# Performance work log

Measured on AMD Instinct MI355X. Metric: run time of the kernel, lower is better.

## Reference

```python
import jax, jax.numpy as jnp
import numpy as np

LMBD = 0.1      # cfg['MODEL']['LAMBDA'][0]
MU = 0.1        # ISTA/FISTA step size (cfg['MODEL']['MU'])
N_STEPS = 4     # cfg['MODEL']['NUM_LAYERS']
FISTA = True    # cfg['MODEL']['ISFISTA']


def _conv(x, W, s, p):
    # torch F.conv2d, NCHW / OIHW
    return jax.lax.conv_general_dilated(x, W, (s, s), [(p, p), (p, p)],
        dimension_numbers=('NCHW', 'OIHW', 'NCHW'))


def _conv_t(z, W, s, p):
    # torch F.conv_transpose2d(z, W, stride=s, padding=p): output (H-1)*s + k - 2p
    k = W.shape[-1]
    Wt = jnp.transpose(jnp.flip(W, (-2, -1)), (1, 0, 2, 3))
    pad = k - 1 - p
    return jax.lax.conv_general_dilated(z, Wt, (1, 1), [(pad, pad), (pad, pad)],
        lhs_dilation=(s, s), dimension_numbers=('NCHW', 'OIHW', 'NCHW'))


def _wnorm(W):
    # per-atom unit-norm dictionary (w_norm=True)
    return W / (jnp.sqrt(jnp.sum(W * W, axis=(1, 2, 3), keepdims=True)) + 1e-12)


def _dict_block(x, W, s, p):
    # unrolled FISTA sparse coding: min_z 0.5||x - W^T*z||^2 + lmbd||z||_1, z>=0
    thr = MU * LMBD
    shrink = lambda u: jax.nn.relu(u - thr)  # non-negative soft threshold
    z0 = shrink(MU * _conv(x, W, s, p))

    def body(carry, _):
        z, z_old, t = carry
        if FISTA:
            t_new = (1.0 + jnp.sqrt(1.0 + 4.0 * t * t)) * 0.5
            y = z + ((t - 1.0) / t_new) * (z - z_old)
        else:
            t_new, y = t, z
        r = x - _conv_t(y, W, s, p)                 # residual in image space
        z_new = shrink(y + MU * _conv(r, W, s, p))  # gradient step + shrinkage
        return (z_new, z, t_new), None

    (z, _, _), _ = jax.lax.scan(body, (z0, z0, jnp.float32(1.0)), None, length=N_STEPS - 1)
    return z


def _bn(x, eps=1e-5):
    # BatchNorm2d at init (gamma=1, beta=0), training-mode batch stats, biased var
    m = jnp.mean(x, axis=(0, 2, 3), keepdims=True)
    v = jnp.var(x, axis=(0, 2, 3), keepdims=True)
    return (x - m) * jax.lax.rsqrt(v + eps)


def _lrelu(x):
    return jnp.where(x >= 0, x, 0.2 * x)


def setup_inputs() -> dict:
    key = jax.random.key(0)
    ks = jax.random.split(key, 7)
    nc, ndf, nz = 3, 64, 128

    def kaiming(k, shape):
        fan_in = shape[1] * shape[2] * shape[3]
        bound = float(np.sqrt(6.0 / fan_in))
        return jax.random.uniform(k, shape, jnp.float32, -bound, bound)

    return {
        'x':  jax.random.normal(ks[0], (64, nc, 96, 96), jnp.float32),
        'W1': kaiming(ks[1], (ndf, nc, 4, 4)),
        'W2': kaiming(ks[2], (ndf * 2, ndf, 4, 4)),
        'W3': kaiming(ks[3], (ndf * 4, ndf * 2, 4, 4)),
        'W4': kaiming(ks[4], (ndf * 8, ndf * 4, 4, 4)),
        'W5': kaiming(ks[5], (ndf * 16, ndf * 8, 4, 4)),
        'W6': kaiming(ks[6], (nz, ndf * 16, 3, 3)),
    }


def reference(x, W1, W2, W3, W4, W5, W6):
    Ws = [_wnorm(w) for w in (W1, W2, W3, W4, W5, W6)]
    # encoder: 96 -> 48 -> 24 -> 12 -> 6 -> 3 -> 1
    o = _lrelu(_dict_block(x, Ws[0], 2, 1))
    for i in range(1, 5):
        o = _lrelu(_bn(_dict_block(o, Ws[i], 2, 1)))
    z = _dict_block(o, Ws[5], 1, 0).reshape(x.shape[0], -1)
    z = z / jnp.maximum(jnp.linalg.norm(z, axis=1, keepdims=True), 1e-12)  # F.normalize
    # decoder (DictConv2d.inverse chain, uses the normalized dictionaries)
    h = z.reshape(z.shape[0], -1, 1, 1)
    h = jax.nn.relu(_bn(_conv_t(h, Ws[5], 1, 0)))
    for i in (4, 3, 2, 1):
        h = jax.nn.relu(_bn(_conv_t(h, Ws[i], 2, 1)))
    x_hat = jnp.tanh(_conv_t(h, Ws[0], 2, 1))
    return z, x_hat
```

## Files before the change

### kernel.cpp

```cpp
#include <hip/hip_runtime.h>
#include <math.h>

#define BLK 256
static constexpr float MU_F  = 0.1f;
static constexpr float THR_F = 0.01f;

typedef __attribute__((ext_vector_type(8))) short bf16x8;
typedef __attribute__((ext_vector_type(4))) float f32x4;

__device__ inline unsigned short f2bf(float f) {
    unsigned u = __float_as_uint(f);
    unsigned r = (u + 0x7fffu + ((u >> 16) & 1u)) >> 16;
    return (unsigned short)r;
}
__device__ inline float bf2f(unsigned short h) {
    return __uint_as_float(((unsigned)h) << 16);
}

__device__ inline float blk_reduce(float v) {
    __shared__ float sh[BLK];
    int tid = threadIdx.x;
    sh[tid] = v;
    __syncthreads();
    #pragma unroll
    for (int s = BLK / 2; s > 0; s >>= 1) {
        if (tid < s) sh[tid] += sh[tid + s];
        __syncthreads();
    }
    float r = sh[0];
    __syncthreads();
    return r;
}

__global__ __launch_bounds__(BLK) void wnorm_pack(
    const float* __restrict__ W, float* __restrict__ Wkc,
    float* __restrict__ Wnout, int Mout, int asz)
{
    int o = blockIdx.x;
    const float* w = W + (size_t)o * asz;
    float s = 0.f;
    for (int i = threadIdx.x; i < asz; i += BLK) { float v = w[i]; s = fmaf(v, v, s); }
    float tot = blk_reduce(s);
    float inv = 1.0f / (sqrtf(tot) + 1e-12f);
    for (int i = threadIdx.x; i < asz; i += BLK) {
        float v = w[i] * inv;
        Wkc[(size_t)i * Mout + o] = v;
        if (Wnout) Wnout[(size_t)o * asz + i] = v;
    }
}

__global__ __launch_bounds__(BLK) void wnorm_pack_bf16(
    const float* __restrict__ W, short* __restrict__ Cpk, short* __restrict__ Tpk,
    int Cout, int Cin)
{
    int o = blockIdx.x;
    int asz = Cin * 16;
    const float* w = W + (size_t)o * asz;
    float s = 0.f;
    for (int i = threadIdx.x; i < asz; i += BLK) { float v = w[i]; s = fmaf(v, v, s); }
    float tot = blk_reduce(s);
    float inv = 1.0f / (sqrtf(tot) + 1e-12f);
    size_t cTot = (size_t)Cout * asz;
    size_t parStride = (size_t)Cout * 4 * Cin;
    size_t tTot = 4 * parStride;
    for (int i = threadIdx.x; i < asz; i += BLK) {
        float v = w[i] * inv;
        unsigned short hb = f2bf(v);
        unsigned short lb = f2bf(v - bf2f(hb));
        size_t cidx = ((size_t)(i >> 3)) * (Cout * 8) + o * 8 + (i & 7);
        Cpk[cidx] = (short)hb;
        Cpk[cTot + cidx] = (short)lb;
        int c = i >> 4, tap = i & 15, kh = tap >> 2, kw = tap & 3;
        int par = (1 - (kh & 1)) * 2 + (1 - (kw & 1));
        int tt = ((kh >> 1) << 1) | (kw >> 1);
        int q = o * 4 + tt;
        size_t tidx = (size_t)par * parStride + ((size_t)(q >> 3)) * (Cin * 8) + c * 8 + (q & 7);
        Tpk[tidx] = (short)hb;
        Tpk[tTot + tidx] = (short)lb;
    }
}

__device__ inline void xcd_remap(int& bx, int& by, int& bz) {
    int nx = gridDim.x, ny = gridDim.y;
    int nwg = nx * ny * gridDim.z;
    int orig = blockIdx.x + nx * (blockIdx.y + ny * blockIdx.z);
    int q8 = nwg >> 3, r8 = nwg & 7, xcd = orig & 7, sidx = orig >> 3;
    int w = (xcd < r8 ? xcd * (q8 + 1) : r8 * (q8 + 1) + (xcd - r8) * q8) + sidx;
    bx = w % nx; int t = w / nx; by = t % ny; bz = t / ny;
}

__global__ __launch_bounds__(BLK) void conv_gemm_bf16(
    const short* __restrict__ Wpk, const float* __restrict__ x,
    const float* __restrict__ yin, float* __restrict__ out,
    int M, int Cx, int Hx, int Wx, int Hout, int Wout,
    int kchunk, int emode)
{
    __shared__ __align__(16) short Wh[4][64][8];
    __shared__ __align__(16) short Wo_[4][64][8];
    __shared__ __align__(16) short Xh[4][64][8];
    __shared__ __align__(16) short Xo[4][64][8];
    int bx, by, bz; xcd_remap(bx, by, bz);
    int tid = threadIdx.x, lane = tid & 63, wid = tid >> 6;
    int HW = Hout * Wout, HWx = Hx * Wx;
    int pbase = bx * 64, m0 = by * 64, kb = bz * kchunk;
    size_t loOff = (size_t)Cx * 16 * M;

    int spl = tid & 63, skb = tid >> 6;
    int sp = pbase + spl;
    int sn = sp / HW; int srr = sp - sn * HW;
    int sho = srr / Wout, swo = srr - sho * Wout;
    const float* xs = x + (size_t)sn * Cx * HWx;
    int h0 = sho * 2 - 1, w0 = swo * 2 - 1;

    int t16 = (skb & 1) * 8;
    int offs[8]; bool valt[8];
    #pragma unroll
    for (int jj = 0; jj < 8; ++jj) {
        int tap = t16 + jj;
        int kh = tap >> 2, kw = tap & 3;
        int h = h0 + kh, w = w0 + kw;
        valt[jj] = ((unsigned)h < (unsigned)Hx) && ((unsigned)w < (unsigned)Wx);
        offs[jj] = h * Wx + w;
    }
    const float* xc = xs + ((size_t)(kb >> 4) + (skb >> 1)) * HWx;

    size_t so = ((size_t)((kb >> 3) + skb)) * (M * 8) + (size_t)m0 * 8 + spl * 8;
    float4 w_hi = *(const float4*)(Wpk + so);
    float4 w_lo = *(const float4*)(Wpk + loOff + so);
    float g[8];
    #pragma unroll
    for (int jj = 0; jj < 8; ++jj) g[jj] = valt[jj] ? xc[offs[jj]] : 0.f;
    xc += 2 * HWx;

    f32x4 acc[4] = {};
    for (int k0 = kb; k0 < kb + kchunk; k0 += 32) {
        *(float4*)(&Wh[skb][spl][0])  = w_hi;
        *(float4*)(&Wo_[skb][spl][0]) = w_lo;
        {
            union { short s8[8]; float4 f; } uh, ul;
            #pragma unroll
            for (int jj = 0; jj < 8; ++jj) {
                float gg = g[jj];
                unsigned short hb = (unsigned short)(__float_as_uint(gg) >> 16);
                uh.s8[jj] = (short)hb;
                ul.s8[jj] = (short)f2bf(gg - bf2f(hb));
            }
            *(float4*)(&Xh[skb][spl][0]) = uh.f;
            *(float4*)(&Xo[skb][spl][0]) = ul.f;
        }
        __syncthreads();
        if (k0 + 32 < kb + kchunk) {
            size_t so2 = ((size_t)(((k0 + 32) >> 3) + skb)) * (M * 8) + (size_t)m0 * 8 + spl * 8;
            w_hi = *(const float4*)(Wpk + so2);
            w_lo = *(const float4*)(Wpk + loOff + so2);
            #pragma unroll
            for (int jj = 0; jj < 8; ++jj) g[jj] = valt[jj] ? xc[offs[jj]] : 0.f;
            xc += 2 * HWx;
        }
        bf16x8 ah = *(const bf16x8*)(&Wh[lane >> 4][wid * 16 + (lane & 15)][0]);
        bf16x8 al = *(const bf16x8*)(&Wo_[lane >> 4][wid * 16 + (lane & 15)][0]);
        #pragma unroll
        for (int nf = 0; nf < 4; ++nf) {
            bf16x8 bh = *(const bf16x8*)(&Xh[lane >> 4][nf * 16 + (lane & 15)][0]);
            bf16x8 bl = *(const bf16x8*)(&Xo[lane >> 4][nf * 16 + (lane & 15)][0]);
            acc[nf] = __builtin_amdgcn_mfma_f32_16x16x32_bf16(al, bh, acc[nf], 0, 0, 0);
            acc[nf] = __builtin_amdgcn_mfma_f32_16x16x32_bf16(ah, bl, acc[nf], 0, 0, 0);
            acc[nf] = __builtin_amdgcn_mfma_f32_16x16x32_bf16(ah, bh, acc[nf], 0, 0, 0);
        }
        __syncthreads();
    }
    int colp = lane & 15, rquad = lane >> 4;
    #pragma unroll
    for (int nf = 0; nf < 4; ++nf) {
        int p = pbase + nf * 16 + colp;
        int n = p / HW; int rr = p - n * HW;
        int ho = rr / Wout, wo = rr - ho * Wout;
        #pragma unroll
        for (int r = 0; r < 4; ++r) {
            int m = m0 + wid * 16 + rquad * 4 + r;
            size_t idx = (((size_t)n * M + m) * Hout + ho) * Wout + wo;
            float v = acc[nf][r];
            if (emode == 0)      out[idx] = fmaxf(MU_F * v - THR_F, 0.f);
            else if (emode == 1) out[idx] = fmaxf(yin[idx] + MU_F * v - THR_F, 0.f);
            else                 atomicAdd(&out[idx], v);
        }
    }
}

__global__ __launch_bounds__(BLK) void convt_gemm_bf16(
    const short* __restrict__ Wpk, const float* __restrict__ z,
    const float* __restrict__ aux, float* __restrict__ out,
    int M, int Cz, int Hz, int Wz, int Ho, int Wo, int emode, int SK)
{
    __shared__ __align__(16) short Wh[4][64][8];
    __shared__ __align__(16) short Wo_[4][64][8];
    __shared__ __align__(16) short Xh[4][64][8];
    __shared__ __align__(16) short Xo[4][64][8];
    int bx, by, bz; xcd_remap(bx, by, bz);
    int tid = threadIdx.x, lane = tid & 63, wid = tid >> 6;
    int par = bz / SK, chunk = bz - par * SK;
    int hbit = par >> 1, wbit = par & 1;
    int czs = Cz / SK;
    int qb = chunk * czs * 4;
    size_t parS = (size_t)Cz * 4 * M;
    const short* Wp = Wpk + (size_t)par * parS;
    size_t loOff = 4 * parS;
    int Hc = Ho >> 1, Wc = Wo >> 1, HWc = Hc * Wc;
    int pbase = bx * 64, m0 = by * 64;

    int spl = tid & 63, skb = tid >> 6;
    int sp = pbase + spl;
    int sn = sp / HWc; int srr = sp - sn * HWc;
    int shc = srr / Wc, swc = srr - shc * Wc;
    int HWz = Hz * Wz;
    const float* zs = z + (size_t)sn * Cz * HWz;

    int offt[4]; bool valt[4];
    #pragma unroll
    for (int t = 0; t < 4; ++t) {
        int ti = t >> 1, tj = t & 1;
        int hn = shc + hbit - ti, wn = swc + wbit - tj;
        valt[t] = ((unsigned)hn < (unsigned)Hz) && ((unsigned)wn < (unsigned)Wz);
        offt[t] = hn * Wz + wn;
    }
    const float* zc = zs + ((size_t)(qb >> 2) + skb * 2) * HWz;

    size_t so = ((size_t)((qb >> 3) + skb)) * (M * 8) + (size_t)m0 * 8 + spl * 8;
    float4 w_hi = *(const float4*)(Wp + so);
    float4 w_lo = *(const float4*)(Wp + loOff + so);
    float g[8];
    #pragma unroll
    for (int jj = 0; jj < 8; ++jj) {
        int t = jj & 3;
        g[jj] = valt[t] ? zc[(jj >> 2) * HWz + offt[t]] : 0.f;
    }
    zc += 8 * HWz;

    f32x4 acc[4] = {};
    for (int q0 = qb; q0 < qb + czs * 4; q0 += 32) {
        *(float4*)(&Wh[skb][spl][0])  = w_hi;
        *(float4*)(&Wo_[skb][spl][0]) = w_lo;
        {
            union { short s8[8]; float4 f; } uh, ul;
            #pragma unroll
            for (int jj = 0; jj < 8; ++jj) {
                float gg = g[jj];
                unsigned short hb = (unsigned short)(__float_as_uint(gg) >> 16);
                uh.s8[jj] = (short)hb;
                ul.s8[jj] = (short)f2bf(gg - bf2f(hb));
            }
            *(float4*)(&Xh[skb][spl][0]) = uh.f;
            *(float4*)(&Xo[skb][spl][0]) = ul.f;
        }
        __syncthreads();
        if (q0 + 32 < qb + czs * 4) {
            size_t so2 = ((size_t)(((q0 + 32) >> 3) + skb)) * (M * 8) + (size_t)m0 * 8 + spl * 8;
            w_hi = *(const float4*)(Wp + so2);
            w_lo = *(const float4*)(Wp + loOff + so2);
            #pragma unroll
            for (int jj = 0; jj < 8; ++jj) {
                int t = jj & 3;
                g[jj] = valt[t] ? zc[(jj >> 2) * HWz + offt[t]] : 0.f;
            }
            zc += 8 * HWz;
        }
        bf16x8 ah = *(const bf16x8*)(&Wh[lane >> 4][wid * 16 + (lane & 15)][0]);
        bf16x8 al = *(const bf16x8*)(&Wo_[lane >> 4][wid * 16 + (lane & 15)][0]);
        #pragma unroll
        for (int nf = 0; nf < 4; ++nf) {
            bf16x8 bh = *(const bf16x8*)(&Xh[lane >> 4][nf * 16 + (lane & 15)][0]);
            bf16x8 bl = *(const bf16x8*)(&Xo[lane >> 4][nf * 16 + (lane & 15)][0]);
            acc[nf] = __builtin_amdgcn_mfma_f32_16x16x32_bf16(al, bh, acc[nf], 0, 0, 0);
            acc[nf] = __builtin_amdgcn_mfma_f32_16x16x32_bf16(ah, bl, acc[nf], 0, 0, 0);
            acc[nf] = __builtin_amdgcn_mfma_f32_16x16x32_bf16(ah, bh, acc[nf], 0, 0, 0);
        }
        __syncthreads();
    }
    int colp = lane & 15, rquad = lane >> 4;
    #pragma unroll
    for (int nf = 0; nf < 4; ++nf) {
        int p = pbase + nf * 16 + colp;
        int n = p / HWc; int rr = p - n * HWc;
        int hc = rr / Wc, wc = rr - hc * Wc;
        int ho = 2 * hc + hbit, wo = 2 * wc + wbit;
        #pragma unroll
        for (int r = 0; r < 4; ++r) {
            int m = m0 + wid * 16 + rquad * 4 + r;
            size_t idx = (((size_t)n * M + m) * Ho + ho) * Wo + wo;
            float v = acc[nf][r];
            if (emode == 0)      out[idx] = aux[idx] - v;
            else if (emode == 1) out[idx] = v;
            else                 atomicAdd(&out[idx], v);
        }
    }
}

template <int KK, int Kk, int S, int P>
__global__ __launch_bounds__(BLK) void conv_gemm(
    const float* __restrict__ Wp, const float* __restrict__ x,
    const float* __restrict__ yin, float* __restrict__ out,
    int M, int Ktot, int Cx, int Hx, int Wx, int Hout, int Wout,
    int kchunk, int emode)
{
    __shared__ float Wt[16][64];
    __shared__ float Xt[16][64];
    int tid = threadIdx.x, tx = tid & 15, ty = tid >> 4;
    int HW = Hout * Wout, HWx = Hx * Wx;
    int pbase = blockIdx.x * 64 + tx * 4;
    int n_[4], ho_[4], wo_[4];
    const float* xb_[4];
    #pragma unroll
    for (int j = 0; j < 4; ++j) {
        int p = pbase + j; int n = p / HW; int r = p - n * HW;
        int ho = r / Wout; int wo = r - ho * Wout;
        n_[j] = n; ho_[j] = ho; wo_[j] = wo;
        xb_[j] = x + (size_t)n * Cx * HWx;
    }
    int m0 = blockIdx.y * 64;
    int kb = blockIdx.z * kchunk, ke = kb + kchunk;
    if (ke > Ktot) ke = Ktot;
    float acc[4][4] = {};
    for (int k0 = kb; k0 < ke; k0 += 16) {
        int kr = k0 + ty;
        *(float4*)&Wt[ty][tx * 4] = *(const float4*)&Wp[(size_t)kr * M + m0 + tx * 4];
        int ci = kr / KK; int t = kr - ci * KK; int kh = t / Kk; int kw = t - kh * Kk;
        int cio = ci * HWx;
        float g[4];
        #pragma unroll
        for (int j = 0; j < 4; ++j) {
            int h = ho_[j] * S - P + kh, w = wo_[j] * S - P + kw;
            g[j] = ((unsigned)h < (unsigned)Hx && (unsigned)w < (unsigned)Wx)
                 ? xb_[j][cio + h * Wx + w] : 0.f;
        }
        *(float4*)&Xt[ty][tx * 4] = make_float4(g[0], g[1], g[2], g[3]);
        __syncthreads();
        #pragma unroll
        for (int kk = 0; kk < 16; ++kk) {
            float4 a = *(float4*)&Wt[kk][ty * 4];
            float4 b = *(float4*)&Xt[kk][tx * 4];
            float aa[4] = {a.x, a.y, a.z, a.w};
            float bb[4] = {b.x, b.y, b.z, b.w};
            #pragma unroll
            for (int i = 0; i < 4; ++i)
                #pragma unroll
                for (int j = 0; j < 4; ++j)
                    acc[i][j] = fmaf(aa[i], bb[j], acc[i][j]);
        }
        __syncthreads();
    }
    #pragma unroll
    for (int i = 0; i < 4; ++i) {
        int m = m0 + ty * 4 + i;
        #pragma unroll
        for (int j = 0; j < 4; ++j) {
            size_t idx = (((size_t)n_[j] * M + m) * Hout + ho_[j]) * Wout + wo_[j];
            float v = acc[i][j];
            if (emode == 0)      out[idx] = fmaxf(MU_F * v - THR_F, 0.f);
            else if (emode == 1) out[idx] = fmaxf(yin[idx] + MU_F * v - THR_F, 0.f);
            else                 atomicAdd(&out[idx], v);
        }
    }
}

__global__ __launch_bounds__(BLK) void outer_gemm(
    const float* __restrict__ Wp, const float* __restrict__ zin,
    const float* __restrict__ aux, float* __restrict__ out,
    int M, int Kz, int emode)
{
    __shared__ float Wt[16][64];
    __shared__ float Xt[16][64];
    int tid = threadIdx.x, tx = tid & 15, ty = tid >> 4;
    int m0 = blockIdx.y * 64;
    float acc[4][4] = {};
    for (int k0 = 0; k0 < Kz; k0 += 16) {
        int kr = k0 + ty;
        *(float4*)&Wt[ty][tx * 4] = *(const float4*)&Wp[(size_t)kr * M + m0 + tx * 4];
        float g[4];
        #pragma unroll
        for (int j = 0; j < 4; ++j) g[j] = zin[(size_t)(tx * 4 + j) * Kz + kr];
        *(float4*)&Xt[ty][tx * 4] = make_float4(g[0], g[1], g[2], g[3]);
        __syncthreads();
        #pragma unroll
        for (int kk = 0; kk < 16; ++kk) {
            float4 a = *(float4*)&Wt[kk][ty * 4];
            float4 b = *(float4*)&Xt[kk][tx * 4];
            float aa[4] = {a.x, a.y, a.z, a.w};
            float bb[4] = {b.x, b.y, b.z, b.w};
            #pragma unroll
            for (int i = 0; i < 4; ++i)
                #pragma unroll
                for (int j = 0; j < 4; ++j)
                    acc[i][j] = fmaf(aa[i], bb[j], acc[i][j]);
        }
        __syncthreads();
    }
    #pragma unroll
    for (int i = 0; i < 4; ++i) {
        int m = m0 + ty * 4 + i;
        #pragma unroll
        for (int j = 0; j < 4; ++j) {
            int n = tx * 4 + j;
            size_t idx = (size_t)n * M + m;
            float v = acc[i][j];
            out[idx] = (emode == 0) ? (aux[idx] - v) : v;
        }
    }
}

__global__ __launch_bounds__(BLK) void convt_m3(
    const float* __restrict__ Wkc0, const float* __restrict__ z,
    const float* __restrict__ aux, float* __restrict__ out,
    int Cz, int Hz, int Wz, int Ho, int Wo, int emode)
{
    __shared__ float Wl[64 * 4 * 3];
    int tid = threadIdx.x;
    int hbit = blockIdx.z >> 1, wbit = blockIdx.z & 1;
    int khp = 1 - hbit, kwp = 1 - wbit;
    int Ktot = Cz * 4;
    for (int kidx = tid; kidx < Ktot; kidx += BLK) {
        int cz = kidx >> 2, t = kidx & 3, ti = t >> 1, tj = t & 1;
        int tap = (khp + 2 * ti) * 4 + (kwp + 2 * tj);
        Wl[kidx * 3 + 0] = Wkc0[(0 * 16 + tap) * 64 + cz];
        Wl[kidx * 3 + 1] = Wkc0[(1 * 16 + tap) * 64 + cz];
        Wl[kidx * 3 + 2] = Wkc0[(2 * 16 + tap) * 64 + cz];
    }
    __syncthreads();
    int Hc = Ho >> 1, Wc = Wo >> 1, HWc = Hc * Wc;
    int p = blockIdx.x * BLK + tid;
    int n = p / HWc, r = p - n * HWc, hc = r / Wc, wc = r - (r / Wc) * Wc;
    const float* zb = z + (size_t)n * Cz * Hz * Wz;
    int offs[4]; bool val[4];
    #pragma unroll
    for (int t = 0; t < 4; ++t) {
        int ti = t >> 1, tj = t & 1;
        int hn = hc + hbit - ti, wn = wc + wbit - tj;
        val[t] = ((unsigned)hn < (unsigned)Hz) && ((unsigned)wn < (unsigned)Wz);
        offs[t] = hn * Wz + wn;
    }
    float a0 = 0.f, a1 = 0.f, a2 = 0.f;
    int HWz = Hz * Wz;
    for (int cz = 0; cz < Cz; ++cz) {
        const float* base = zb + cz * HWz;
        #pragma unroll
        for (int t = 0; t < 4; ++t) {
            float g = val[t] ? base[offs[t]] : 0.f;
            int wi = (cz * 4 + t) * 3;
            a0 = fmaf(g, Wl[wi + 0], a0);
            a1 = fmaf(g, Wl[wi + 1], a1);
            a2 = fmaf(g, Wl[wi + 2], a2);
        }
    }
    int ho = 2 * hc + hbit, wo = 2 * wc + wbit;
    #pragma unroll
    for (int u = 0; u < 3; ++u) {
        float v = (u == 0) ? a0 : (u == 1) ? a1 : a2;
        size_t idx = (((size_t)n * 3 + u) * Ho + ho) * Wo + wo;
        out[idx] = (emode == 0) ? (aux[idx] - v) : tanhf(v);
    }
}

__global__ __launch_bounds__(BLK) void shrink_epi_v4(
    const float* __restrict__ p, const float* __restrict__ y,
    float* __restrict__ o, int n4, int mode)
{
    int i = blockIdx.x * BLK + threadIdx.x;
    if (i >= n4) return;
    float4 pv = ((const float4*)p)[i];
    float4 r;
    if (mode == 1) {
        float4 yv = ((const float4*)y)[i];
        r.x = fmaxf(yv.x + MU_F * pv.x - THR_F, 0.f);
        r.y = fmaxf(yv.y + MU_F * pv.y - THR_F, 0.f);
        r.z = fmaxf(yv.z + MU_F * pv.z - THR_F, 0.f);
        r.w = fmaxf(yv.w + MU_F * pv.w - THR_F, 0.f);
    } else {
        r.x = fmaxf(MU_F * pv.x - THR_F, 0.f);
        r.y = fmaxf(MU_F * pv.y - THR_F, 0.f);
        r.z = fmaxf(MU_F * pv.z - THR_F, 0.f);
        r.w = fmaxf(MU_F * pv.w - THR_F, 0.f);
    }
    ((float4*)o)[i] = r;
}

__global__ __launch_bounds__(BLK) void res_epi_v4(
    const float* __restrict__ aux, const float* __restrict__ acc,
    float* __restrict__ o, int n4)
{
    int i = blockIdx.x * BLK + threadIdx.x;
    if (i >= n4) return;
    float4 a = ((const float4*)aux)[i];
    float4 b = ((const float4*)acc)[i];
    ((float4*)o)[i] = make_float4(a.x - b.x, a.y - b.y, a.z - b.z, a.w - b.w);
}

__global__ __launch_bounds__(BLK) void y_update_v4(
    const float* __restrict__ z, const float* __restrict__ zo,
    float* __restrict__ y, int n4, float c)
{
    int i = blockIdx.x * BLK + threadIdx.x;
    if (i >= n4) return;
    float4 zv = ((const float4*)z)[i];
    float4 ov = ((const float4*)zo)[i];
    ((float4*)y)[i] = make_float4(
        fmaf(c, zv.x - ov.x, zv.x), fmaf(c, zv.y - ov.y, zv.y),
        fmaf(c, zv.z - ov.z, zv.z), fmaf(c, zv.w - ov.w, zv.w));
}

__global__ __launch_bounds__(BLK) void bn_stats_part(
    const float* __restrict__ x, float* __restrict__ stats,
    int N, int C, int HW, int nblk)
{
    int c = blockIdx.x, b = blockIdx.y;
    int cnt = N * HW;
    float s = 0.f, s2 = 0.f;
    for (int i = b * BLK + threadIdx.x; i < cnt; i += nblk * BLK) {
        int n = i / HW, hw = i - n * HW;
        float v = x[((size_t)n * C + c) * HW + hw];
        s += v; s2 = fmaf(v, v, s2);
    }
    float ts  = blk_reduce(s);
    float ts2 = blk_reduce(s2);
    if (threadIdx.x == 0) {
        atomicAdd(&stats[c], ts);
        atomicAdd(&stats[C + c], ts2);
    }
}
__global__ __launch_bounds__(BLK) void bn_finalize(
    const float* __restrict__ stats, float* __restrict__ mean,
    float* __restrict__ rstd, int C, int cnt)
{
    int c = blockIdx.x * BLK + threadIdx.x;
    if (c >= C) return;
    float m = stats[c] / cnt;
    float var = stats[C + c] / cnt - m * m;
    mean[c] = m;
    rstd[c] = rsqrtf(var + 1e-5f);
}

__global__ __launch_bounds__(BLK) void bn_act_v4(
    const float* __restrict__ x, const float* __restrict__ mean,
    const float* __restrict__ rstd, float* __restrict__ out,
    int n4, int C, int HW, int use_bn, int act)
{
    int i = blockIdx.x * BLK + threadIdx.x;
    if (i >= n4) return;
    float4 v = ((const float4*)x)[i];
    float e[4] = {v.x, v.y, v.z, v.w};
    int base = i * 4;
    #pragma unroll
    for (int j = 0; j < 4; ++j) {
        float t = e[j];
        if (use_bn) { int c = ((base + j) / HW) % C; t = (t - mean[c]) * rstd[c]; }
        e[j] = (act == 0) ? ((t >= 0.f) ? t : 0.2f * t) : fmaxf(t, 0.f);
    }
    ((float4*)out)[i] = make_float4(e[0], e[1], e[2], e[3]);
}

__global__ __launch_bounds__(128) void rownorm_kernel(
    const float* __restrict__ z, float* __restrict__ out, float* __restrict__ zvec)
{
    __shared__ float sh[128];
    int r = blockIdx.x, tid = threadIdx.x;
    float v = z[r * 128 + tid];
    sh[tid] = v * v;
    __syncthreads();
    #pragma unroll
    for (int s = 64; s > 0; s >>= 1) {
        if (tid < s) sh[tid] += sh[tid + s];
        __syncthreads();
    }
    float nrm = fmaxf(sqrtf(sh[0]), 1e-12f);
    float o = v / nrm;
    out[r * 128 + tid] = o;
    zvec[r * 128 + tid] = o;
}

static inline int gdiv(int a, int b) { return (a + b - 1) / b; }

extern "C" void kernel_launch(void* const* d_in, const int* in_sizes, int n_in,
                              void* d_out, int out_size, void* d_ws, size_t ws_size,
                              hipStream_t stream)
{
    const float* x = (const float*)d_in[0];
    const float* W[6];
    for (int i = 0; i < 6; ++i) W[i] = (const float*)d_in[1 + i];
    float* ws  = (float*)d_ws;
    float* out = (float*)d_out;

    const int Cin[6]  = {3, 64, 128, 256, 512, 1024};
    const int Cout[6] = {64, 128, 256, 512, 1024, 128};
    const int Hin[6]  = {96, 48, 24, 12, 6, 3};
    const int Hout[6] = {48, 24, 12, 6, 3, 1};
    const int N = 64;
    const int SKc[6] = {1, 1, 2, 4, 8, 1};
    const int SKt[6] = {1, 1, 1, 2, 4, 1};

    size_t off = 0;
    float* Wkc0 = ws + off; off += 3072;
    float* Wkc5 = ws + off; off += 1179648;
    float* Wn5  = ws + off; off += 1179648;
    const size_t csz[5] = {0, 131072, 524288, 2097152, 8388608};
    short* Cpk[5]; short* Tpk[5];
    {
        short* sbase = (short*)(ws + off);
        size_t soff = 0;
        for (int L = 1; L < 5; ++L) { Cpk[L] = sbase + soff; soff += 2 * csz[L]; }
        for (int L = 1; L < 5; ++L) { Tpk[L] = sbase + soff; soff += 2 * csz[L]; }
        off += soff / 2;
    }
    const size_t POOL = 30081024;
    float* pool = ws + off; off += POOL;
    float* xb   = ws + off; off += 9437184;
    float* mean = ws + off; off += 1024;
    float* rstd = ws + off; off += 1024;
    float* stats= ws + off; off += 2048;
    float* zvec = ws + off; off += 8192;
    float* pbuf = ws + off; off += 2359296;

    wnorm_pack<<<64, BLK, 0, stream>>>(W[0], Wkc0, nullptr, 64, 48);
    for (int L = 1; L < 5; ++L)
        wnorm_pack_bf16<<<Cout[L], BLK, 0, stream>>>(W[L], Cpk[L], Tpk[L], Cout[L], Cin[L]);
    wnorm_pack<<<128, BLK, 0, stream>>>(W[5], Wkc5, Wn5, 128, 9216);

    double td = 1.0; float cc[3];
    for (int i = 0; i < 3; ++i) {
        double tn = (1.0 + sqrt(1.0 + 4.0 * td * td)) * 0.5;
        cc[i] = (float)((td - 1.0) / tn);
        td = tn;
    }

    auto run_bn_stats = [&](const float* src, int C, int HW) {
        int cnt = N * HW;
        int nblk = 2048 / C; if (nblk < 1) nblk = 1;
        int maxb = gdiv(cnt, BLK); if (nblk > maxb) nblk = maxb;
        hipMemsetAsync(stats, 0, 2 * C * sizeof(float), stream);
        bn_stats_part<<<dim3(C, nblk), BLK, 0, stream>>>(src, stats, N, C, HW, nblk);
        bn_finalize<<<gdiv(C, BLK), BLK, 0, stream>>>(stats, mean, rstd, C, cnt);
    };

    const float* in = x;
    for (int L = 0; L < 6; ++L) {
        int zTot = N * Cout[L] * Hout[L] * Hout[L];
        int xTot = N * Cin[L] * Hin[L] * Hin[L];
        int npix = N * Hout[L] * Hout[L];
        dim3 ge4(gdiv(zTot / 4, BLK));
        dim3 gr4(gdiv(xTot / 4, BLK));

        float* zA = pool;
        float* zB = pool + (size_t)zTot;
        float* yb = pool + (size_t)2 * zTot;
        float* rb = pool + (size_t)3 * zTot;

        auto launch_conv = [&](const float* src, const float* y, float* dst, int mode) {
            if (L == 5) {
                hipMemsetAsync(pbuf, 0, (size_t)zTot * 4, stream);
                conv_gemm<9, 3, 1, 0><<<dim3(1, 2, 72), BLK, 0, stream>>>(Wkc5, src,
                    nullptr, pbuf, 128, 9216, 1024, 3, 3, 1, 1, 128, 2);
                shrink_epi_v4<<<gdiv(zTot / 4, BLK), BLK, 0, stream>>>(pbuf, y, dst, zTot / 4, mode);
            } else if (L == 0) {
                conv_gemm<16, 4, 2, 1><<<dim3(npix / 64, 1), BLK, 0, stream>>>(
                    Wkc0, src, y, dst, 64, 48, 3, 96, 96, 48, 48, 48, mode);
            } else if (SKc[L] == 1) {
                conv_gemm_bf16<<<dim3(npix / 64, Cout[L] / 64), BLK, 0, stream>>>(
                    Cpk[L], src, y, dst, Cout[L], Cin[L], Hin[L], Hin[L],
                    Hout[L], Hout[L], Cin[L] * 16, mode);
            } else {
                int sk = SKc[L];
                hipMemsetAsync(pbuf, 0, (size_t)zTot * 4, stream);
                conv_gemm_bf16<<<dim3(npix / 64, Cout[L] / 64, sk), BLK, 0, stream>>>(
                    Cpk[L], src, nullptr, pbuf, Cout[L], Cin[L], Hin[L], Hin[L],
                    Hout[L], Hout[L], Cin[L] * 16 / sk, 2);
                shrink_epi_v4<<<gdiv(zTot / 4, BLK), BLK, 0, stream>>>(pbuf, y, dst, zTot / 4, mode);
            }
        };

        launch_conv(in, nullptr, zA, 0);

        float* z = zA; float* zo = zB;
        for (int it = 0; it < 3; ++it) {
            const float* ybp;
            if (it == 0) {
                ybp = z;
            } else {
                y_update_v4<<<ge4, BLK, 0, stream>>>(z, zo, yb, zTot / 4, cc[it]);
                ybp = yb;
            }
            if (L == 0) {
                convt_m3<<<dim3(N * 48 * 48 / BLK, 1, 4), BLK, 0, stream>>>(
                    Wkc0, ybp, in, rb, 64, 48, 48, 96, 96, 0);
            } else if (L < 5) {
                int xpixc = N * (Hin[L] / 2) * (Hin[L] / 2);
                int sk = SKt[L];
                if (sk == 1) {
                    convt_gemm_bf16<<<dim3(xpixc / 64, Cin[L] / 64, 4), BLK, 0, stream>>>(
                        Tpk[L], ybp, in, rb, Cin[L], Cout[L], Hout[L], Hout[L],
                        Hin[L], Hin[L], 0, 1);
                } else {
                    hipMemsetAsync(rb, 0, (size_t)xTot * 4, stream);
                    convt_gemm_bf16<<<dim3(xpixc / 64, Cin[L] / 64, 4 * sk), BLK, 0, stream>>>(
                        Tpk[L], ybp, nullptr, rb, Cin[L], Cout[L], Hout[L], Hout[L],
                        Hin[L], Hin[L], 2, sk);
                    res_epi_v4<<<gr4, BLK, 0, stream>>>(in, rb, rb, xTot / 4);
                }
            } else {
                outer_gemm<<<dim3(1, 144), BLK, 0, stream>>>(Wn5, ybp, in, rb, 9216, 128, 0);
            }
            launch_conv(rb, ybp, zo, 1);
            float* tmp = z; z = zo; zo = tmp;
        }

        int HW = Hout[L] * Hout[L];
        if (L == 0) {
            bn_act_v4<<<ge4, BLK, 0, stream>>>(z, nullptr, nullptr, xb, zTot / 4, Cout[L], HW, 0, 0);
            in = xb;
        } else if (L < 5) {
            run_bn_stats(z, Cout[L], HW);
            bn_act_v4<<<ge4, BLK, 0, stream>>>(z, mean, rstd, xb, zTot / 4, Cout[L], HW, 1, 0);
            in = xb;
        } else {
            rownorm_kernel<<<64, 128, 0, stream>>>(z, out, zvec);
        }
    }

    float* zA = pool;
    float* zB = pool + 9437184;
    {
        int oT = N * 1024 * 9;
        outer_gemm<<<dim3(1, 144), BLK, 0, stream>>>(Wn5, zvec, nullptr, zA, 9216, 128, 1);
        run_bn_stats(zA, 1024, 9);
        bn_act_v4<<<gdiv(oT / 4, BLK), BLK, 0, stream>>>(zA, mean, rstd, zB, oT / 4, 1024, 9, 1, 1);
    }
    float* cur = zB;
    for (int i = 4; i >= 1; --i) {
        int oT = N * Cin[i] * Hin[i] * Hin[i];
        int xpixc = N * (Hin[i] / 2) * (Hin[i] / 2);
        int sk = SKt[i];
        if (sk == 1) {
            convt_gemm_bf16<<<dim3(xpixc / 64, Cin[i] / 64, 4), BLK, 0, stream>>>(
                Tpk[i], cur, nullptr, zA, Cin[i], Cout[i], Hout[i], Hout[i],
                Hin[i], Hin[i], 1, 1);
        } else {
            hipMemsetAsync(zA, 0, (size_t)oT * 4, stream);
            convt_gemm_bf16<<<dim3(xpixc / 64, Cin[i] / 64, 4 * sk), BLK, 0, stream>>>(
                Tpk[i], cur, nullptr, zA, Cin[i], Cout[i], Hout[i], Hout[i],
                Hin[i], Hin[i], 2, sk);
        }
        run_bn_stats(zA, Cin[i], Hin[i] * Hin[i]);
        bn_act_v4<<<gdiv(oT / 4, BLK), BLK, 0, stream>>>(zA, mean, rstd, zB, oT / 4,
            Cin[i], Hin[i] * Hin[i], 1, 1);
        cur = zB;
    }
    convt_m3<<<dim3(N * 48 * 48 / BLK, 1, 4), BLK, 0, stream>>>(
        Wkc0, cur, nullptr, out + 8192, 64, 48, 48, 96, 96, 2);
}
```

Baseline: 3.582 ms.

## Process 64-wide K slices per iteration in conv and conv-transpose GEMMs

```diff
diff --git a/kernel.cpp b/kernel.cpp
--- a/kernel.cpp
+++ b/kernel.cpp
@@ -95,10 +95,10 @@
     int M, int Cx, int Hx, int Wx, int Hout, int Wout,
     int kchunk, int emode)
 {
-    __shared__ __align__(16) short Wh[4][64][8];
-    __shared__ __align__(16) short Wo_[4][64][8];
-    __shared__ __align__(16) short Xh[4][64][8];
-    __shared__ __align__(16) short Xo[4][64][8];
+    __shared__ __align__(16) short Wh[8][64][8];
+    __shared__ __align__(16) short Wo_[8][64][8];
+    __shared__ __align__(16) short Xh[8][64][8];
+    __shared__ __align__(16) short Xo[8][64][8];
     int bx, by, bz; xcd_remap(bx, by, bz);
     int tid = threadIdx.x, lane = tid & 63, wid = tid >> 6;
     int HW = Hout * Wout, HWx = Hx * Wx;
@@ -124,48 +124,62 @@
     }
     const float* xc = xs + ((size_t)(kb >> 4) + (skb >> 1)) * HWx;
 
-    size_t so = ((size_t)((kb >> 3) + skb)) * (M * 8) + (size_t)m0 * 8 + spl * 8;
-    float4 w_hi = *(const float4*)(Wpk + so);
-    float4 w_lo = *(const float4*)(Wpk + loOff + so);
-    float g[8];
-    #pragma unroll
-    for (int jj = 0; jj < 8; ++jj) g[jj] = valt[jj] ? xc[offs[jj]] : 0.f;
-    xc += 2 * HWx;
+    float4 w_hi[2], w_lo[2];
+    float g[2][8];
+    #pragma unroll
+    for (int h = 0; h < 2; ++h) {
+        size_t so = ((size_t)(((kb + 32 * h) >> 3) + skb)) * (M * 8) + (size_t)m0 * 8 + spl * 8;
+        w_hi[h] = *(const float4*)(Wpk + so);
+        w_lo[h] = *(const float4*)(Wpk + loOff + so);
+        #pragma unroll
+        for (int jj = 0; jj < 8; ++jj)
+            g[h][jj] = valt[jj] ? xc[h * 2 * HWx + offs[jj]] : 0.f;
+    }
+    xc += 4 * HWx;
 
     f32x4 acc[4] = {};
-    for (int k0 = kb; k0 < kb + kchunk; k0 += 32) {
-        *(float4*)(&Wh[skb][spl][0])  = w_hi;
-        *(float4*)(&Wo_[skb][spl][0]) = w_lo;
-        {
+    for (int k0 = kb; k0 < kb + kchunk; k0 += 64) {
+        #pragma unroll
+        for (int h = 0; h < 2; ++h) {
+            *(float4*)(&Wh[h * 4 + skb][spl][0])  = w_hi[h];
+            *(float4*)(&Wo_[h * 4 + skb][spl][0]) = w_lo[h];
             union { short s8[8]; float4 f; } uh, ul;
             #pragma unroll
             for (int jj = 0; jj < 8; ++jj) {
-                float gg = g[jj];
+                float gg = g[h][jj];
                 unsigned short hb = (unsigned short)(__float_as_uint(gg) >> 16);
                 uh.s8[jj] = (short)hb;
                 ul.s8[jj] = (short)f2bf(gg - bf2f(hb));
             }
-            *(float4*)(&Xh[skb][spl][0]) = uh.f;
-            *(float4*)(&Xo[skb][spl][0]) = ul.f;
-        }
-        __syncthreads();
-        if (k0 + 32 < kb + kchunk) {
-            size_t so2 = ((size_t)(((k0 + 32) >> 3) + skb)) * (M * 8) + (size_t)m0 * 8 + spl * 8;
-            w_hi = *(const float4*)(Wpk + so2);
-            w_lo = *(const float4*)(Wpk + loOff + so2);
+            *(float4*)(&Xh[h * 4 + skb][spl][0]) = uh.f;
+            *(float4*)(&Xo[h * 4 + skb][spl][0]) = ul.f;
+        }
+        __syncthreads();
+        if (k0 + 64 < kb + kchunk) {
             #pragma unroll
-            for (int jj = 0; jj < 8; ++jj) g[jj] = valt[jj] ? xc[offs[jj]] : 0.f;
-            xc += 2 * HWx;
-        }
-        bf16x8 ah = *(const bf16x8*)(&Wh[lane >> 4][wid * 16 + (lane & 15)][0]);
-        bf16x8 al = *(const bf16x8*)(&Wo_[lane >> 4][wid * 16 + (lane & 15)][0]);
-        #pragma unroll
-        for (int nf = 0; nf < 4; ++nf) {
-            bf16x8 bh = *(const bf16x8*)(&Xh[lane >> 4][nf * 16 + (lane & 15)][0]);
-            bf16x8 bl = *(const bf16x8*)(&Xo[lane >> 4][nf * 16 + (lane & 15)][0]);
-            acc[nf] = __builtin_amdgcn_mfma_f32_16x16x32_bf16(al, bh, acc[nf], 0, 0, 0);
-            acc[nf] = __builtin_amdgcn_mfma_f32_16x16x32_bf16(ah, bl, acc[nf], 0, 0, 0);
-            acc[nf] = __builtin_amdgcn_mfma_f32_16x16x32_bf16(ah, bh, acc[nf], 0, 0, 0);
+            for (int h = 0; h < 2; ++h) {
+                size_t so2 = ((size_t)(((k0 + 64 + 32 * h) >> 3) + skb)) * (M * 8)
+                           + (size_t)m0 * 8 + spl * 8;
+                w_hi[h] = *(const float4*)(Wpk + so2);
+                w_lo[h] = *(const float4*)(Wpk + loOff + so2);
+                #pragma unroll
+                for (int jj = 0; jj < 8; ++jj)
+                    g[h][jj] = valt[jj] ? xc[h * 2 * HWx + offs[jj]] : 0.f;
+            }
+            xc += 4 * HWx;
+        }
+        #pragma unroll
+        for (int half = 0; half < 2; ++half) {
+            bf16x8 ah = *(const bf16x8*)(&Wh[half * 4 + (lane >> 4)][wid * 16 + (lane & 15)][0]);
+            bf16x8 al = *(const bf16x8*)(&Wo_[half * 4 + (lane >> 4)][wid * 16 + (lane & 15)][0]);
+            #pragma unroll
+            for (int nf = 0; nf < 4; ++nf) {
+                bf16x8 bh = *(const bf16x8*)(&Xh[half * 4 + (lane >> 4)][nf * 16 + (lane & 15)][0]);
+                bf16x8 bl = *(const bf16x8*)(&Xo[half * 4 + (lane >> 4)][nf * 16 + (lane & 15)][0]);
+                acc[nf] = __builtin_amdgcn_mfma_f32_16x16x32_bf16(al, bh, acc[nf], 0, 0, 0);
+                acc[nf] = __builtin_amdgcn_mfma_f32_16x16x32_bf16(ah, bl, acc[nf], 0, 0, 0);
+                acc[nf] = __builtin_amdgcn_mfma_f32_16x16x32_bf16(ah, bh, acc[nf], 0, 0, 0);
+            }
         }
         __syncthreads();
     }
@@ -192,10 +206,10 @@
     const float* __restrict__ aux, float* __restrict__ out,
     int M, int Cz, int Hz, int Wz, int Ho, int Wo, int emode, int SK)
 {
-    __shared__ __align__(16) short Wh[4][64][8];
-    __shared__ __align__(16) short Wo_[4][64][8];
-    __shared__ __align__(16) short Xh[4][64][8];
-    __shared__ __align__(16) short Xo[4][64][8];
+    __shared__ __align__(16) short Wh[8][64][8];
+    __shared__ __align__(16) short Wo_[8][64][8];
+    __shared__ __align__(16) short Xh[8][64][8];
+    __shared__ __align__(16) short Xo[8][64][8];
     int bx, by, bz; xcd_remap(bx, by, bz);
     int tid = threadIdx.x, lane = tid & 63, wid = tid >> 6;
     int par = bz / SK, chunk = bz - par * SK;
@@ -225,54 +239,66 @@
     }
     const float* zc = zs + ((size_t)(qb >> 2) + skb * 2) * HWz;
 
-    size_t so = ((size_t)((qb >> 3) + skb)) * (M * 8) + (size_t)m0 * 8 + spl * 8;
-    float4 w_hi = *(const float4*)(Wp + so);
-    float4 w_lo = *(const float4*)(Wp + loOff + so);
-    float g[8];
-    #pragma unroll
-    for (int jj = 0; jj < 8; ++jj) {
-        int t = jj & 3;
-        g[jj] = valt[t] ? zc[(jj >> 2) * HWz + offt[t]] : 0.f;
-    }
-    zc += 8 * HWz;
+    float4 w_hi[2], w_lo[2];
+    float g[2][8];
+    #pragma unroll
+    for (int h = 0; h < 2; ++h) {
+        size_t so = ((size_t)(((qb + 32 * h) >> 3) + skb)) * (M * 8) + (size_t)m0 * 8 + spl * 8;
+        w_hi[h] = *(const float4*)(Wp + so);
+        w_lo[h] = *(const float4*)(Wp + loOff + so);
+        #pragma unroll
+        for (int jj = 0; jj < 8; ++jj) {
+            int t = jj & 3;
+            g[h][jj] = valt[t] ? zc[(h * 8 + (jj >> 2)) * HWz + offt[t]] : 0.f;
+        }
+    }
+    zc += 16 * HWz;
 
     f32x4 acc[4] = {};
-    for (int q0 = qb; q0 < qb + czs * 4; q0 += 32) {
-        *(float4*)(&Wh[skb][spl][0])  = w_hi;
-        *(float4*)(&Wo_[skb][spl][0]) = w_lo;
-        {
+    for (int q0 = qb; q0 < qb + czs * 4; q0 += 64) {
+        #pragma unroll
+        for (int h = 0; h < 2; ++h) {
+            *(float4*)(&Wh[h * 4 + skb][spl][0])  = w_hi[h];
+            *(float4*)(&Wo_[h * 4 + skb][spl][0]) = w_lo[h];
             union { short s8[8]; float4 f; } uh, ul;
             #pragma unroll
             for (int jj = 0; jj < 8; ++jj) {
-                float gg = g[jj];
+                float gg = g[h][jj];
                 unsigned short hb = (unsigned short)(__float_as_uint(gg) >> 16);
                 uh.s8[jj] = (short)hb;
                 ul.s8[jj] = (short)f2bf(gg - bf2f(hb));
             }
-            *(float4*)(&Xh[skb][spl][0]) = uh.f;
-            *(float4*)(&Xo[skb][spl][0]) = ul.f;
-        }
-        __syncthreads();
-        if (q0 + 32 < qb + czs * 4) {
-            size_t so2 = ((size_t)(((q0 + 32) >> 3) + skb)) * (M * 8) + (size_t)m0 * 8 + spl * 8;
-            w_hi = *(const float4*)(Wp + so2);
-            w_lo = *(const float4*)(Wp + loOff + so2);
+            *(float4*)(&Xh[h * 4 + skb][spl][0]) = uh.f;
+            *(float4*)(&Xo[h * 4 + skb][spl][0]) = ul.f;
+        }
+        __syncthreads();
+        if (q0 + 64 < qb + czs * 4) {
             #pragma unroll
-            for (int jj = 0; jj < 8; ++jj) {
-                int t = jj & 3;
-                g[jj] = valt[t] ? zc[(jj >> 2) * HWz + offt[t]] : 0.f;
-            }
-            zc += 8 * HWz;
-        }
-        bf16x8 ah = *(const bf16x8*)(&Wh[lane >> 4][wid * 16 + (lane & 15)][0]);
-        bf16x8 al = *(const bf16x8*)(&Wo_[lane >> 4][wid * 16 + (lane & 15)][0]);
-        #pragma unroll
-        for (int nf = 0; nf < 4; ++nf) {
-            bf16x8 bh = *(const bf16x8*)(&Xh[lane >> 4][nf * 16 + (lane & 15)][0]);
-            bf16x8 bl = *(const bf16x8*)(&Xo[lane >> 4][nf * 16 + (lane & 15)][0]);
-            acc[nf] = __builtin_amdgcn_mfma_f32_16x16x32_bf16(al, bh, acc[nf], 0, 0, 0);
-            acc[nf] = __builtin_amdgcn_mfma_f32_16x16x32_bf16(ah, bl, acc[nf], 0, 0, 0);
-            acc[nf] = __builtin_amdgcn_mfma_f32_16x16x32_bf16(ah, bh, acc[nf], 0, 0, 0);
+            for (int h = 0; h < 2; ++h) {
+                size_t so2 = ((size_t)(((q0 + 64 + 32 * h) >> 3) + skb)) * (M * 8)
+                           + (size_t)m0 * 8 + spl * 8;
+                w_hi[h] = *(const float4*)(Wp + so2);
+                w_lo[h] = *(const float4*)(Wp + loOff + so2);
+                #pragma unroll
+                for (int jj = 0; jj < 8; ++jj) {
+                    int t = jj & 3;
+                    g[h][jj] = valt[t] ? zc[(h * 8 + (jj >> 2)) * HWz + offt[t]] : 0.f;
+                }
+            }
+            zc += 16 * HWz;
+        }
+        #pragma unroll
+        for (int half = 0; half < 2; ++half) {
+            bf16x8 ah = *(const bf16x8*)(&Wh[half * 4 + (lane >> 4)][wid * 16 + (lane & 15)][0]);
+            bf16x8 al = *(const bf16x8*)(&Wo_[half * 4 + (lane >> 4)][wid * 16 + (lane & 15)][0]);
+            #pragma unroll
+            for (int nf = 0; nf < 4; ++nf) {
+                bf16x8 bh = *(const bf16x8*)(&Xh[half * 4 + (lane >> 4)][nf * 16 + (lane & 15)][0]);
+                bf16x8 bl = *(const bf16x8*)(&Xo[half * 4 + (lane >> 4)][nf * 16 + (lane & 15)][0]);
+                acc[nf] = __builtin_amdgcn_mfma_f32_16x16x32_bf16(al, bh, acc[nf], 0, 0, 0);
+                acc[nf] = __builtin_amdgcn_mfma_f32_16x16x32_bf16(ah, bl, acc[nf], 0, 0, 0);
+                acc[nf] = __builtin_amdgcn_mfma_f32_16x16x32_bf16(ah, bh, acc[nf], 0, 0, 0);
+            }
         }
         __syncthreads();
     }
```

New measurement: 5.569 ms. +55.5%, slower.
